# Kernel tuning notes

Measured on AMD Instinct MI355X. Metric: run time of the kernel, lower is better.

## Reference

```python
import jax, jax.numpy as jnp
import numpy as np

WD, WH, WW = 4, 8, 8
N_WIN = WD * WH * WW  # 256 tokens per window
NUM_HEADS = 8
DIM = 512
HIDDEN = int(DIM * 4.0)
SHIFT = (2, 4, 4)
EPS = 1e-5


def _rel_pos_index():
    coords = np.stack(np.meshgrid(np.arange(WD), np.arange(WH), np.arange(WW), indexing='ij'))
    cf = coords.reshape(3, -1)  # [3, N]
    rc = cf[:, :, None] - cf[:, None, :]  # [3, N, N]
    rc = rc.transpose(1, 2, 0).astype(np.int64)
    rc[:, :, 0] += WD - 1
    rc[:, :, 1] += WH - 1
    rc[:, :, 2] += WW - 1
    rc[:, :, 0] *= (2 * WH - 1) * (2 * WW - 1)
    rc[:, :, 1] *= (2 * WW - 1)
    return jnp.asarray(rc.sum(-1))  # [N, N]

REL_IDX = _rel_pos_index()


def setup_inputs() -> dict:
    key = jax.random.key(0)
    ks = jax.random.split(key, 10)
    B, D, H, W = 1, 16, 64, 64
    L = D * H * W
    s = 0.02
    table_size = (2 * WD - 1) * (2 * WH - 1) * (2 * WW - 1)  # 1575
    return {
        'x': jax.random.normal(ks[0], (B, L, DIM), jnp.float32),
        't_emb': jax.random.normal(ks[1], (B, DIM), jnp.float32),
        'ada_w': jax.random.normal(ks[2], (DIM, 6 * DIM), jnp.float32) * s,
        'ada_b': jnp.zeros((6 * DIM,), jnp.float32),
        'rel_table': jax.random.normal(ks[3], (table_size, NUM_HEADS), jnp.float32) * s,
        'qkv_w': jax.random.normal(ks[4], (DIM, 3 * DIM), jnp.float32) * s,
        'qkv_b': jnp.zeros((3 * DIM,), jnp.float32),
        'proj_w': jax.random.normal(ks[5], (DIM, DIM), jnp.float32) * s,
        'proj_b': jnp.zeros((DIM,), jnp.float32),
        'fc1_w': jax.random.normal(ks[6], (DIM, HIDDEN), jnp.float32) * s,
        'fc1_b': jnp.zeros((HIDDEN,), jnp.float32),
        'fc2_w': jax.random.normal(ks[7], (HIDDEN, DIM), jnp.float32) * s,
        'fc2_b': jnp.zeros((DIM,), jnp.float32),
        'D': D, 'H': H, 'W': W,
    }


def _layernorm(y):
    m = jnp.mean(y, axis=-1, keepdims=True)
    v = jnp.mean(jnp.square(y - m), axis=-1, keepdims=True)
    return (y - m) * jax.lax.rsqrt(v + EPS)


def _window_partition(x3, D, H, W):
    B, _, _, _, C = x3.shape
    x3 = x3.reshape(B, D // WD, WD, H // WH, WH, W // WW, WW, C)
    x3 = x3.transpose(0, 1, 3, 5, 2, 4, 6, 7)
    return x3.reshape(-1, N_WIN, C)


def _window_reverse(win, B, D, H, W):
    C = win.shape[-1]
    x3 = win.reshape(B, D // WD, H // WH, W // WW, WD, WH, WW, C)
    x3 = x3.transpose(0, 1, 4, 2, 5, 3, 6, 7)
    return x3.reshape(B, D, H, W, C)


def _window_attention(xn, rel_table, qkv_w, qkv_b, proj_w, proj_b):
    Bn, N, C = xn.shape
    h, d = NUM_HEADS, C // NUM_HEADS
    qkv = (xn @ qkv_w + qkv_b).reshape(Bn, N, 3, h, d).transpose(2, 0, 3, 1, 4)
    q, k, v = qkv[0], qkv[1], qkv[2]
    scale = d ** -0.5
    attn = jnp.einsum('bhnd,bhmd->bhnm', q * scale, k)  # [Bn, h, N, N]
    bias = rel_table[REL_IDX]  # gather -> [N, N, h]
    attn = jax.nn.softmax(attn + bias.transpose(2, 0, 1)[None], axis=-1)
    o = jnp.einsum('bhnm,bhmd->bhnd', attn, v)
    o = o.transpose(0, 2, 1, 3).reshape(Bn, N, C)
    return o @ proj_w + proj_b


def reference(x, t_emb, ada_w, ada_b, rel_table, qkv_w, qkv_b, proj_w, proj_b,
              fc1_w, fc1_b, fc2_w, fc2_b, D, H, W):
    B, L, C = x.shape
    mod = jax.nn.silu(t_emb) @ ada_w + ada_b  # [B, 6C]
    shift_msa, scale_msa, gate_msa, shift_mlp, scale_mlp, gate_mlp = jnp.split(mod, 6, axis=-1)

    x3 = x.reshape(B, D, H, W, C)
    x3 = jnp.roll(x3, shift=(-SHIFT[0], -SHIFT[1], -SHIFT[2]), axis=(1, 2, 3))
    xw = _window_partition(x3, D, H, W)  # [B*nW, N, C]

    xn = _layernorm(xw) * (1.0 + scale_msa[:, None, :]) + shift_msa[:, None, :]
    attn_out = _window_attention(xn, rel_table, qkv_w, qkv_b, proj_w, proj_b)
    xw = xw + gate_msa[:, None, :] * attn_out

    x3 = _window_reverse(xw, B, D, H, W)
    x3 = jnp.roll(x3, shift=SHIFT, axis=(1, 2, 3))
    x = x3.reshape(B, L, C)

    xn = _layernorm(x) * (1.0 + scale_mlp[:, None, :]) + shift_mlp[:, None, :]
    h1 = jax.nn.gelu(xn @ fc1_w + fc1_b, approximate=False)
    mlp_out = h1 @ fc2_w + fc2_b
    return x + gate_mlp[:, None, :] * mlp_out
```

## Files before the change

### kernel.cpp

```cpp
#include <hip/hip_runtime.h>
#include <hip/hip_bf16.h>
#include <math.h>


typedef __attribute__((ext_vector_type(8))) short short8;
typedef __attribute__((ext_vector_type(4))) short bs4;
typedef __attribute__((ext_vector_type(4))) float f32x4;

typedef const __attribute__((address_space(1))) unsigned int gu32;
typedef __attribute__((address_space(3))) unsigned int lu32;

__device__ __forceinline__ float bf2f(short s) {
  unsigned int u = ((unsigned int)(unsigned short)s) << 16;
  float f;
  __builtin_memcpy(&f, &u, 4);
  return f;
}
__device__ __forceinline__ short f2bf(float f) {
  unsigned int u;
  __builtin_memcpy(&u, &f, 4);
  u += 0x7FFFu + ((u >> 16) & 1u);
  return (short)(u >> 16);
}
__device__ __forceinline__ short f2bf_trunc(float f) {
  unsigned int u;
  __builtin_memcpy(&u, &f, 4);
  return (short)(u >> 16);
}

__device__ __forceinline__ int win_to_src(int p) {
  int wi = p >> 8, t = p & 255;
  int sd = (((wi >> 6) << 2) + (t >> 6) + 2) & 15;
  int sh = ((((wi >> 3) & 7) << 3) + ((t >> 3) & 7) + 4) & 63;
  int sw = (((wi & 7) << 3) + (t & 7) + 4) & 63;
  return (sd << 12) | (sh << 6) | sw;
}

__global__ __launch_bounds__(256) void mod_kernel(
    const float* __restrict__ t_emb, const float* __restrict__ ada_w,
    const float* __restrict__ ada_b, float* __restrict__ mod) {
  __shared__ float sl[512];
  int tid = threadIdx.x;
  for (int r = 0; r < 2; ++r) {
    float x = t_emb[r * 256 + tid];
    sl[r * 256 + tid] = x / (1.f + expf(-x));
  }
  __syncthreads();
  int col = blockIdx.x * 256 + tid;
  float acc = ada_b[col];
  for (int k = 0; k < 512; ++k)
    acc += sl[k] * ada_w[(size_t)k * 3072 + col];
  mod[col] = acc;
}

__global__ __launch_bounds__(256) void bias_kernel(
    const float* __restrict__ rel_table, short* __restrict__ biasT) {
  int head = blockIdx.x >> 8;
  int j = blockIdx.x & 255;
  int i = threadIdx.x;
  int di = i >> 6, hi = (i >> 3) & 7, wi = i & 7;
  int dj = j >> 6, hj = (j >> 3) & 7, wj = j & 7;
  int idx = (di - dj + 3) * 225 + (hi - hj + 7) * 15 + (wi - wj + 7);
  biasT[(size_t)blockIdx.x * 256 + i] = f2bf(rel_table[idx * 8 + head]);
}

__global__ __launch_bounds__(256) void perm_transpose_kernel(
    const float* __restrict__ in, short* __restrict__ out, int Nin, int K) {
  __shared__ float t[64][65];
  int a = blockIdx.x;
  int kb = blockIdx.y;
  int tx = threadIdx.x & 63, ty = threadIdx.x >> 6;
#pragma unroll
  for (int r = 0; r < 16; ++r) {
    int kk = ty * 16 + r;
    t[kk][tx] = in[(size_t)(kb * 64 + kk) * Nin + a * 64 + tx];
  }
  __syncthreads();
#pragma unroll
  for (int r = 0; r < 16; ++r) {
    int jl = ty * 16 + r;
    int lc = 4 * (jl & 15) + ((jl >> 4) & 3);
    out[(size_t)(a * 64 + jl) * K + kb * 64 + tx] = f2bf(t[tx][lc]);
  }
}

template <int GATHER>
__global__ __launch_bounds__(256) void ln_kernel(
    const float* __restrict__ xin, short* __restrict__ xout,
    const float* __restrict__ shv, const float* __restrict__ scv) {
  int wave = threadIdx.x >> 6, lane = threadIdx.x & 63;
  int p = blockIdx.x * 4 + wave;
  int s = GATHER ? win_to_src(p) : p;
  const f32x4* px = (const f32x4*)(xin + (size_t)s * 512 + lane * 8);
  f32x4 a = px[0], b = px[1];
  float xs[8];
#pragma unroll
  for (int j = 0; j < 4; ++j) { xs[j] = a[j]; xs[4 + j] = b[j]; }
  float sum = 0.f, sq = 0.f;
#pragma unroll
  for (int j = 0; j < 8; ++j) { sum += xs[j]; sq += xs[j] * xs[j]; }
#pragma unroll
  for (int off = 1; off < 64; off <<= 1) {
    sum += __shfl_xor(sum, off, 64);
    sq += __shfl_xor(sq, off, 64);
  }
  float mean = sum * (1.f / 512.f);
  float var = sq * (1.f / 512.f) - mean * mean;
  float rs = rsqrtf(var + 1e-5f);
  short8 o;
#pragma unroll
  for (int j = 0; j < 8; ++j) {
    int c = lane * 8 + j;
    float val = (xs[j] - mean) * rs * (1.f + scv[c]) + shv[c];
    o[j] = f2bf(val);
  }
  *(short8*)(xout + (size_t)p * 512 + lane * 8) = o;
}

template <int EPI>
__global__ __launch_bounds__(512) void gemm_kernel(
    const short* __restrict__ A, const short* __restrict__ BT,
    const float* __restrict__ bias, void* __restrict__ Cv,
    int M, int N, int K, int nbn,
    const float* __restrict__ resid, const float* __restrict__ gate) {
  __shared__ __align__(16) short Atl[256 * 64];
  __shared__ __align__(16) short Btl[128 * 64];

  int nwg = gridDim.x;
  int bid = blockIdx.x;
  int q = nwg >> 3, r = nwg & 7;
  int xcd = bid & 7, idx = bid >> 3;
  int swz = (xcd < r ? xcd * (q + 1) : r * (q + 1) + (xcd - r) * q) + idx;
  int bm = swz / nbn, bn = swz % nbn;

  int tid = threadIdx.x;
  int lane = tid & 63, wave = tid >> 6;
  int l15 = lane & 15, lg = lane >> 4;
  int wr = (wave >> 1) * 64, wc = (wave & 1) * 64;

  const size_t rowb = (size_t)K * 2;
  const char* ga[4];
  const char* gb[2];
  int loA[4], loB[2];
#pragma unroll
  for (int rr = 0; rr < 4; ++rr) {
    int o = rr * 8192 + tid * 16;
    int so = o ^ (((o >> 7) & 7) << 4);
    int row = so >> 7, cb = so & 127;
    loA[rr] = o;
    ga[rr] = (const char*)A + (size_t)(bm * 256 + row) * rowb + cb;
  }
#pragma unroll
  for (int rr = 0; rr < 2; ++rr) {
    int o = rr * 8192 + tid * 16;
    int so = o ^ (((o >> 7) & 7) << 4);
    int row = so >> 7, cb = so & 127;
    loB[rr] = o;
    gb[rr] = (const char*)BT + (size_t)(bn * 128 + row) * rowb + cb;
  }

  f32x4 acc[4][4];
#pragma unroll
  for (int m = 0; m < 4; ++m)
#pragma unroll
    for (int n = 0; n < 4; ++n) acc[m][n] = (f32x4){0.f, 0.f, 0.f, 0.f};

  const int swr = (l15 & 7) << 4;

  for (int kt = 0; kt < K; kt += 64) {
#pragma unroll
    for (int rr = 0; rr < 4; ++rr) {
      __builtin_amdgcn_global_load_lds((gu32*)ga[rr], (lu32*)((char*)Atl + loA[rr]), 16, 0, 0);
      ga[rr] += 128;
    }
#pragma unroll
    for (int rr = 0; rr < 2; ++rr) {
      __builtin_amdgcn_global_load_lds((gu32*)gb[rr], (lu32*)((char*)Btl + loB[rr]), 16, 0, 0);
      gb[rr] += 128;
    }
    __syncthreads();

    short8 af[2][4], bfr[2][4];
#pragma unroll
    for (int m = 0; m < 4; ++m) {
      int base = (wr + m * 16 + l15) * 128;
#pragma unroll
      for (int ks = 0; ks < 2; ++ks)
        af[ks][m] = *(const short8*)((const char*)Atl + base + ((ks * 64 + lg * 16) ^ swr));
    }
#pragma unroll
    for (int n = 0; n < 4; ++n) {
      int base = (wc + n * 16 + l15) * 128;
#pragma unroll
      for (int ks = 0; ks < 2; ++ks)
        bfr[ks][n] = *(const short8*)((const char*)Btl + base + ((ks * 64 + lg * 16) ^ swr));
    }
#pragma unroll
    for (int ks = 0; ks < 2; ++ks)
#pragma unroll
      for (int m = 0; m < 4; ++m)
#pragma unroll
        for (int n = 0; n < 4; ++n)
          acc[m][n] = __builtin_amdgcn_mfma_f32_16x16x32_bf16(af[ks][m], bfr[ks][n], acc[m][n], 0, 0, 0);
    __syncthreads();
  }

  int colb = bn * 128 + wc + 4 * l15;
  f32x4 bv4 = *(const f32x4*)(bias + colb);
  if (EPI == 0) {
    float sc = (colb < 512) ? 0.125f : 1.f;
#pragma unroll
    for (int m = 0; m < 4; ++m)
#pragma unroll
      for (int i = 0; i < 4; ++i) {
        int row = bm * 256 + wr + m * 16 + lg * 4 + i;
        bs4 pk;
#pragma unroll
        for (int n = 0; n < 4; ++n) pk[n] = f2bf_trunc((acc[m][n][i] + bv4[n]) * sc);
        *(bs4*)((short*)Cv + (size_t)row * N + colb) = pk;
      }
  } else if (EPI == 1) {
#pragma unroll
    for (int m = 0; m < 4; ++m)
#pragma unroll
      for (int i = 0; i < 4; ++i) {
        int row = bm * 256 + wr + m * 16 + lg * 4 + i;
        bs4 pk;
#pragma unroll
        for (int n = 0; n < 4; ++n) {
          float v = acc[m][n][i] + bv4[n];
          float tt = v * (0.7978845608f + 0.0356774081f * v * v);
          float sg = 1.f / (1.f + __expf(-2.f * tt));
          pk[n] = f2bf_trunc(v * sg);
        }
        *(bs4*)((short*)Cv + (size_t)row * N + colb) = pk;
      }
  } else {
    f32x4 gv = *(const f32x4*)(gate + colb);
#pragma unroll
    for (int m = 0; m < 4; ++m)
#pragma unroll
      for (int i = 0; i < 4; ++i) {
        int row = bm * 256 + wr + m * 16 + lg * 4 + i;
        int s = (EPI == 2) ? win_to_src(row) : row;
        f32x4 rv = *(const f32x4*)(resid + (size_t)s * 512 + colb);
        f32x4 o;
#pragma unroll
        for (int n = 0; n < 4; ++n) o[n] = rv[n] + gv[n] * (acc[m][n][i] + bv4[n]);
        *(f32x4*)((float*)Cv + (size_t)s * 512 + colb) = o;
      }
  }
}

__global__ __launch_bounds__(512) void attn_kernel(
    const short* __restrict__ qkv, const short* __restrict__ biasT,
    short* __restrict__ aout) {
  __shared__ __align__(16) short vt[64][264];
  __shared__ __align__(16) short pl[8][32][40];
  int win = blockIdx.x, head = blockIdx.y;
  int tid = threadIdx.x, lane = tid & 63, wave = tid >> 6;
  int l15 = lane & 15, lg = lane >> 4;
  const short* qp = qkv + (size_t)win * 256 * 1536 + head * 64;
  const short* kp = qp + 512;
  const short* vp = qp + 1024;

  int key = tid >> 1, dh = (tid & 1) * 32;
#pragma unroll
  for (int r = 0; r < 4; ++r) {
    short8 vv = *(const short8*)(vp + (size_t)key * 1536 + dh + r * 8);
#pragma unroll
    for (int j = 0; j < 8; ++j) vt[dh + r * 8 + j][key] = vv[j];
  }

  short8 qf[2][2];
#pragma unroll
  for (int m = 0; m < 2; ++m)
#pragma unroll
    for (int kk = 0; kk < 2; ++kk)
      qf[m][kk] = *(const short8*)(qp + (size_t)(wave * 32 + m * 16 + l15) * 1536 + kk * 32 + lg * 8);

  __syncthreads();

  float lsum[2][4];
  f32x4 ao[2][4];
#pragma unroll
  for (int m = 0; m < 2; ++m)
#pragma unroll
    for (int i = 0; i < 4; ++i) lsum[m][i] = 0.f;
#pragma unroll
  for (int m = 0; m < 2; ++m)
#pragma unroll
    for (int n = 0; n < 4; ++n) ao[m][n] = (f32x4){0.f, 0.f, 0.f, 0.f};

  for (int kc = 0; kc < 4; ++kc) {
    f32x4 sv[2][4];
#pragma unroll
    for (int m = 0; m < 2; ++m)
#pragma unroll
      for (int n = 0; n < 4; ++n) sv[m][n] = (f32x4){0.f, 0.f, 0.f, 0.f};
#pragma unroll
    for (int n = 0; n < 4; ++n)
#pragma unroll
      for (int kk = 0; kk < 2; ++kk) {
        short8 kf = *(const short8*)(kp + (size_t)(kc * 64 + n * 16 + l15) * 1536 + kk * 32 + lg * 8);
#pragma unroll
        for (int m = 0; m < 2; ++m)
          sv[m][n] = __builtin_amdgcn_mfma_f32_16x16x32_bf16(qf[m][kk], kf, sv[m][n], 0, 0, 0);
      }
#pragma unroll
    for (int n = 0; n < 4; ++n) {
      const short* bq = biasT + (size_t)(head * 256 + kc * 64 + n * 16 + l15) * 256 + wave * 32 + lg * 4;
#pragma unroll
      for (int m = 0; m < 2; ++m) {
        bs4 bt = *(const bs4*)(bq + m * 16);
#pragma unroll
        for (int i = 0; i < 4; ++i) {
          float pe = __expf(sv[m][n][i] + bf2f(bt[i]));
          sv[m][n][i] = pe;
          lsum[m][i] += pe;
        }
      }
    }
#pragma unroll
    for (int s = 0; s < 2; ++s) {
#pragma unroll
      for (int m = 0; m < 2; ++m)
#pragma unroll
        for (int nn = 0; nn < 2; ++nn) {
          int n = 2 * s + nn;
#pragma unroll
          for (int i = 0; i < 4; ++i)
            pl[wave][m * 16 + lg * 4 + i][nn * 16 + l15] = f2bf_trunc(sv[m][n][i]);
        }
      short8 pf[2];
#pragma unroll
      for (int m = 0; m < 2; ++m)
        pf[m] = *(const short8*)&pl[wave][m * 16 + l15][lg * 8];
#pragma unroll
      for (int n2 = 0; n2 < 4; ++n2) {
        short8 vf = *(const short8*)&vt[n2 * 16 + l15][kc * 64 + s * 32 + lg * 8];
#pragma unroll
        for (int m = 0; m < 2; ++m)
          ao[m][n2] = __builtin_amdgcn_mfma_f32_16x16x32_bf16(pf[m], vf, ao[m][n2], 0, 0, 0);
      }
    }
  }

#pragma unroll
  for (int m = 0; m < 2; ++m)
#pragma unroll
    for (int i = 0; i < 4; ++i) {
#pragma unroll
      for (int off = 1; off < 16; off <<= 1)
        lsum[m][i] += __shfl_xor(lsum[m][i], off, 64);
    }

#pragma unroll
  for (int m = 0; m < 2; ++m)
#pragma unroll
    for (int i = 0; i < 4; ++i) {
      float inv = 1.f / lsum[m][i];
      int row = win * 256 + wave * 32 + m * 16 + lg * 4 + i;
#pragma unroll
      for (int n = 0; n < 4; ++n)
        aout[(size_t)row * 512 + head * 64 + n * 16 + l15] = f2bf(ao[m][n][i] * inv);
    }
}

extern "C" void kernel_launch(void* const* d_in, const int* in_sizes, int n_in,
                              void* d_out, int out_size, void* d_ws, size_t ws_size,
                              hipStream_t stream) {
  (void)in_sizes; (void)n_in; (void)out_size; (void)ws_size;
  const float* x         = (const float*)d_in[0];
  const float* t_emb     = (const float*)d_in[1];
  const float* ada_w     = (const float*)d_in[2];
  const float* ada_b     = (const float*)d_in[3];
  const float* rel_table = (const float*)d_in[4];
  const float* qkv_w     = (const float*)d_in[5];
  const float* qkv_b     = (const float*)d_in[6];
  const float* proj_w    = (const float*)d_in[7];
  const float* proj_b    = (const float*)d_in[8];
  const float* fc1_w     = (const float*)d_in[9];
  const float* fc1_b     = (const float*)d_in[10];
  const float* fc2_w     = (const float*)d_in[11];
  const float* fc2_b     = (const float*)d_in[12];
  float* out = (float*)d_out;
  char* ws = (char*)d_ws;

  float* mod    = (float*)(ws);
  short* biasT  = (short*)(ws + 16384);
  short* qkvwT  = (short*)(ws + 16384 + 2097152);
  short* projwT = qkvwT + 1536 * 512;
  short* fc1wT  = projwT + 512 * 512;
  short* fc2wT  = fc1wT + 2048 * 512;
  short* xn     = (short*)(ws + 8404992);
  short* qkvb   = xn + (size_t)65536 * 512;
  short* attno  = qkvb + (size_t)65536 * 1536;
  short* h1     = qkvb;
  float* x2     = out;

  mod_kernel<<<12, 256, 0, stream>>>(t_emb, ada_w, ada_b, mod);
  bias_kernel<<<2048, 256, 0, stream>>>(rel_table, biasT);
  perm_transpose_kernel<<<dim3(24, 8), 256, 0, stream>>>(qkv_w, qkvwT, 1536, 512);
  perm_transpose_kernel<<<dim3(8, 8), 256, 0, stream>>>(proj_w, projwT, 512, 512);
  perm_transpose_kernel<<<dim3(32, 8), 256, 0, stream>>>(fc1_w, fc1wT, 2048, 512);
  perm_transpose_kernel<<<dim3(8, 32), 256, 0, stream>>>(fc2_w, fc2wT, 512, 2048);

  ln_kernel<1><<<16384, 256, 0, stream>>>(x, xn, mod + 0, mod + 512);
  gemm_kernel<0><<<256 * 12, 512, 0, stream>>>(xn, qkvwT, qkv_b, qkvb,
                                               65536, 1536, 512, 12, nullptr, nullptr);
  attn_kernel<<<dim3(256, 8), 512, 0, stream>>>(qkvb, biasT, attno);
  gemm_kernel<2><<<256 * 4, 512, 0, stream>>>(attno, projwT, proj_b, x2,
                                              65536, 512, 512, 4, x, mod + 1024);
  ln_kernel<0><<<16384, 256, 0, stream>>>(x2, xn, mod + 1536, mod + 2048);
  gemm_kernel<1><<<256 * 16, 512, 0, stream>>>(xn, fc1wT, fc1_b, h1,
                                               65536, 2048, 512, 16, nullptr, nullptr);
  gemm_kernel<3><<<256 * 4, 512, 0, stream>>>(h1, fc2wT, fc2_b, out,
                                              65536, 512, 2048, 4, x2, mod + 2560);
}
```

Measured before the change: 846.1 us.

## Double-buffer GEMM LDS tiles with K=32 stages and async prefetch

The GEMM main loop now uses two LDS buffers of half the K depth (32 instead of 64). Global-to-LDS loads for tile t+2 are issued while MFMAs run on tile t, with explicit vmcnt/lgkmcnt waits and barriers. This is meant to hide global memory latency behind compute instead of serialising load-then-compute. The cost is smaller k-steps, which means more barriers per unit of work, and a re-derived XOR swizzle for 64-byte rows that may cause LDS bank conflicts.

```diff
diff --git a/kernel.cpp b/kernel.cpp
--- a/kernel.cpp
+++ b/kernel.cpp
@@ -123,8 +123,8 @@
     const float* __restrict__ bias, void* __restrict__ Cv,
     int M, int N, int K, int nbn,
     const float* __restrict__ resid, const float* __restrict__ gate) {
-  __shared__ __align__(16) short Atl[256 * 64];
-  __shared__ __align__(16) short Btl[128 * 64];
+  __shared__ __align__(16) short Atl[2][256 * 32];
+  __shared__ __align__(16) short Btl[2][128 * 32];
 
   int nwg = gridDim.x;
   int bid = blockIdx.x;
@@ -139,24 +139,21 @@
   int wr = (wave >> 1) * 64, wc = (wave & 1) * 64;
 
   const size_t rowb = (size_t)K * 2;
-  const char* ga[4];
-  const char* gb[2];
-  int loA[4], loB[2];
-#pragma unroll
-  for (int rr = 0; rr < 4; ++rr) {
-    int o = rr * 8192 + tid * 16;
-    int so = o ^ (((o >> 7) & 7) << 4);
-    int row = so >> 7, cb = so & 127;
-    loA[rr] = o;
-    ga[rr] = (const char*)A + (size_t)(bm * 256 + row) * rowb + cb;
-  }
+  const char* ga[2];
+  const char* gb;
+  int loA[2], loB;
 #pragma unroll
   for (int rr = 0; rr < 2; ++rr) {
     int o = rr * 8192 + tid * 16;
-    int so = o ^ (((o >> 7) & 7) << 4);
-    int row = so >> 7, cb = so & 127;
-    loB[rr] = o;
-    gb[rr] = (const char*)BT + (size_t)(bn * 128 + row) * rowb + cb;
+    int so = o ^ (((o >> 6) & 3) << 4);
+    loA[rr] = o;
+    ga[rr] = (const char*)A + (size_t)(bm * 256 + (so >> 6)) * rowb + (so & 63);
+  }
+  {
+    int o = tid * 16;
+    int so = o ^ (((o >> 6) & 3) << 4);
+    loB = o;
+    gb = (const char*)BT + (size_t)(bn * 128 + (so >> 6)) * rowb + (so & 63);
   }
 
   f32x4 acc[4][4];
@@ -165,44 +162,60 @@
 #pragma unroll
     for (int n = 0; n < 4; ++n) acc[m][n] = (f32x4){0.f, 0.f, 0.f, 0.f};
 
-  const int swr = (l15 & 7) << 4;
-
-  for (int kt = 0; kt < K; kt += 64) {
-#pragma unroll
-    for (int rr = 0; rr < 4; ++rr) {
-      __builtin_amdgcn_global_load_lds((gu32*)ga[rr], (lu32*)((char*)Atl + loA[rr]), 16, 0, 0);
-      ga[rr] += 128;
-    }
-#pragma unroll
-    for (int rr = 0; rr < 2; ++rr) {
-      __builtin_amdgcn_global_load_lds((gu32*)gb[rr], (lu32*)((char*)Btl + loB[rr]), 16, 0, 0);
-      gb[rr] += 128;
-    }
-    __syncthreads();
-
-    short8 af[2][4], bfr[2][4];
-#pragma unroll
-    for (int m = 0; m < 4; ++m) {
-      int base = (wr + m * 16 + l15) * 128;
-#pragma unroll
-      for (int ks = 0; ks < 2; ++ks)
-        af[ks][m] = *(const short8*)((const char*)Atl + base + ((ks * 64 + lg * 16) ^ swr));
-    }
-#pragma unroll
-    for (int n = 0; n < 4; ++n) {
-      int base = (wc + n * 16 + l15) * 128;
-#pragma unroll
-      for (int ks = 0; ks < 2; ++ks)
-        bfr[ks][n] = *(const short8*)((const char*)Btl + base + ((ks * 64 + lg * 16) ^ swr));
-    }
-#pragma unroll
-    for (int ks = 0; ks < 2; ++ks)
-#pragma unroll
-      for (int m = 0; m < 4; ++m)
-#pragma unroll
-        for (int n = 0; n < 4; ++n)
-          acc[m][n] = __builtin_amdgcn_mfma_f32_16x16x32_bf16(af[ks][m], bfr[ks][n], acc[m][n], 0, 0, 0);
-    __syncthreads();
+  const int swr = (l15 & 3) << 4;
+
+  auto stage = [&](int buf) {
+    __builtin_amdgcn_global_load_lds((gu32*)ga[0], (lu32*)((char*)Atl[buf] + loA[0]), 16, 0, 0);
+    __builtin_amdgcn_global_load_lds((gu32*)ga[1], (lu32*)((char*)Atl[buf] + loA[1]), 16, 0, 0);
+    __builtin_amdgcn_global_load_lds((gu32*)gb,    (lu32*)((char*)Btl[buf] + loB),    16, 0, 0);
+    ga[0] += 64; ga[1] += 64; gb += 64;
+  };
+
+  const int nt = K >> 5;
+  stage(0);
+  stage(1);
+  int c = 0;
+  for (int t = 0; t < nt - 1; ++t) {
+    asm volatile("s_waitcnt vmcnt(3)" ::: "memory");
+    __builtin_amdgcn_sched_barrier(0);
+    __builtin_amdgcn_s_barrier();
+    __builtin_amdgcn_sched_barrier(0);
+    short8 af[4], bfr[4];
+#pragma unroll
+    for (int m = 0; m < 4; ++m)
+      af[m] = *(const short8*)((const char*)Atl[c] + (wr + m * 16 + l15) * 64 + (lg * 16 ^ swr));
+#pragma unroll
+    for (int n = 0; n < 4; ++n)
+      bfr[n] = *(const short8*)((const char*)Btl[c] + (wc + n * 16 + l15) * 64 + (lg * 16 ^ swr));
+    asm volatile("s_waitcnt lgkmcnt(0)" ::: "memory");
+    __builtin_amdgcn_sched_barrier(0);
+    __builtin_amdgcn_s_barrier();
+    __builtin_amdgcn_sched_barrier(0);
+    if (t + 2 < nt) stage(c);
+#pragma unroll
+    for (int m = 0; m < 4; ++m)
+#pragma unroll
+      for (int n = 0; n < 4; ++n)
+        acc[m][n] = __builtin_amdgcn_mfma_f32_16x16x32_bf16(af[m], bfr[n], acc[m][n], 0, 0, 0);
+    c ^= 1;
+  }
+  asm volatile("s_waitcnt vmcnt(0)" ::: "memory");
+  __builtin_amdgcn_sched_barrier(0);
+  __builtin_amdgcn_s_barrier();
+  __builtin_amdgcn_sched_barrier(0);
+  {
+    short8 af[4], bfr[4];
+#pragma unroll
+    for (int m = 0; m < 4; ++m)
+      af[m] = *(const short8*)((const char*)Atl[c] + (wr + m * 16 + l15) * 64 + (lg * 16 ^ swr));
+#pragma unroll
+    for (int n = 0; n < 4; ++n)
+      bfr[n] = *(const short8*)((const char*)Btl[c] + (wc + n * 16 + l15) * 64 + (lg * 16 ^ swr));
+#pragma unroll
+    for (int m = 0; m < 4; ++m)
+#pragma unroll
+      for (int n = 0; n < 4; ++n)
+        acc[m][n] = __builtin_amdgcn_mfma_f32_16x16x32_bf16(af[m], bfr[n], acc[m][n], 0, 0, 0);
   }
 
   int colb = bn * 128 + wc + 4 * l15;
```

Result: slower. 864.4 us (+2.2%).

## Double-buffer GEMM LDS tiles and enlarge block tile to 256x256

Applied to the files above, without the earlier changes.

The GEMM kernel now keeps two LDS buffers and issues global-to-LDS loads for the next K tile while computing the current one, with one barrier per iteration instead of two. The block tile grows from 256x128 to 256x256, so each wave computes a 128x64 sub-tile with 32 accumulators, and the grids are halved to match. This aims to hide load latency and raise data reuse per LDS byte. In exchange it uses 128KB of LDS and more registers per block, which limits occupancy, and the 512-wide GEMMs now launch only 512 blocks.

```diff
diff --git a/kernel.cpp b/kernel.cpp
--- a/kernel.cpp
+++ b/kernel.cpp
@@ -118,13 +118,13 @@
 }
 
 template <int EPI>
-__global__ __launch_bounds__(512) void gemm_kernel(
+__global__ __launch_bounds__(512, 2) void gemm_kernel(
     const short* __restrict__ A, const short* __restrict__ BT,
     const float* __restrict__ bias, void* __restrict__ Cv,
     int M, int N, int K, int nbn,
     const float* __restrict__ resid, const float* __restrict__ gate) {
-  __shared__ __align__(16) short Atl[256 * 64];
-  __shared__ __align__(16) short Btl[128 * 64];
+  __shared__ __align__(16) short Atl[2][256 * 64];
+  __shared__ __align__(16) short Btl[2][256 * 64];
 
   int nwg = gridDim.x;
   int bid = blockIdx.x;
@@ -136,99 +136,109 @@
   int tid = threadIdx.x;
   int lane = tid & 63, wave = tid >> 6;
   int l15 = lane & 15, lg = lane >> 4;
-  int wr = (wave >> 1) * 64, wc = (wave & 1) * 64;
+  int wr = (wave >> 2) * 128;
+  int wc = (wave & 3) * 64;
 
   const size_t rowb = (size_t)K * 2;
   const char* ga[4];
-  const char* gb[2];
-  int loA[4], loB[2];
+  const char* gb[4];
+  int lo[4];
 #pragma unroll
   for (int rr = 0; rr < 4; ++rr) {
     int o = rr * 8192 + tid * 16;
     int so = o ^ (((o >> 7) & 7) << 4);
     int row = so >> 7, cb = so & 127;
-    loA[rr] = o;
+    lo[rr] = o;
     ga[rr] = (const char*)A + (size_t)(bm * 256 + row) * rowb + cb;
-  }
-#pragma unroll
-  for (int rr = 0; rr < 2; ++rr) {
-    int o = rr * 8192 + tid * 16;
-    int so = o ^ (((o >> 7) & 7) << 4);
-    int row = so >> 7, cb = so & 127;
-    loB[rr] = o;
-    gb[rr] = (const char*)BT + (size_t)(bn * 128 + row) * rowb + cb;
-  }
-
-  f32x4 acc[4][4];
-#pragma unroll
-  for (int m = 0; m < 4; ++m)
+    gb[rr] = (const char*)BT + (size_t)(bn * 256 + row) * rowb + cb;
+  }
+
+  f32x4 acc[8][4];
+#pragma unroll
+  for (int m = 0; m < 8; ++m)
 #pragma unroll
     for (int n = 0; n < 4; ++n) acc[m][n] = (f32x4){0.f, 0.f, 0.f, 0.f};
 
   const int swr = (l15 & 7) << 4;
 
-  for (int kt = 0; kt < K; kt += 64) {
+  auto stage = [&](int buf) {
 #pragma unroll
     for (int rr = 0; rr < 4; ++rr) {
-      __builtin_amdgcn_global_load_lds((gu32*)ga[rr], (lu32*)((char*)Atl + loA[rr]), 16, 0, 0);
+      __builtin_amdgcn_global_load_lds((gu32*)ga[rr], (lu32*)((char*)Atl[buf] + lo[rr]), 16, 0, 0);
       ga[rr] += 128;
     }
 #pragma unroll
-    for (int rr = 0; rr < 2; ++rr) {
-      __builtin_amdgcn_global_load_lds((gu32*)gb[rr], (lu32*)((char*)Btl + loB[rr]), 16, 0, 0);
+    for (int rr = 0; rr < 4; ++rr) {
+      __builtin_amdgcn_global_load_lds((gu32*)gb[rr], (lu32*)((char*)Btl[buf] + lo[rr]), 16, 0, 0);
       gb[rr] += 128;
     }
-    __syncthreads();
-
-    short8 af[2][4], bfr[2][4];
-#pragma unroll
-    for (int m = 0; m < 4; ++m) {
-      int base = (wr + m * 16 + l15) * 128;
-#pragma unroll
-      for (int ks = 0; ks < 2; ++ks)
-        af[ks][m] = *(const short8*)((const char*)Atl + base + ((ks * 64 + lg * 16) ^ swr));
-    }
+  };
+
+  const int nt = K >> 6;
+  stage(0);
+  asm volatile("s_waitcnt vmcnt(0)" ::: "memory");
+  __builtin_amdgcn_sched_barrier(0);
+  __builtin_amdgcn_s_barrier();
+  int c = 0;
+  for (int t = 0; t < nt; ++t) {
+    if (t + 1 < nt) stage(c ^ 1);
+    short8 bfr[4][2];
 #pragma unroll
     for (int n = 0; n < 4; ++n) {
       int base = (wc + n * 16 + l15) * 128;
 #pragma unroll
       for (int ks = 0; ks < 2; ++ks)
-        bfr[ks][n] = *(const short8*)((const char*)Btl + base + ((ks * 64 + lg * 16) ^ swr));
-    }
-#pragma unroll
-    for (int ks = 0; ks < 2; ++ks)
-#pragma unroll
-      for (int m = 0; m < 4; ++m)
-#pragma unroll
-        for (int n = 0; n < 4; ++n)
-          acc[m][n] = __builtin_amdgcn_mfma_f32_16x16x32_bf16(af[ks][m], bfr[ks][n], acc[m][n], 0, 0, 0);
-    __syncthreads();
-  }
-
-  int colb = bn * 128 + wc + 4 * l15;
+        bfr[n][ks] = *(const short8*)((const char*)Btl[c] + base + ((ks * 64 + lg * 16) ^ swr));
+    }
+#pragma unroll
+    for (int mh = 0; mh < 2; ++mh) {
+      short8 af[4][2];
+#pragma unroll
+      for (int m = 0; m < 4; ++m) {
+        int base = (wr + mh * 64 + m * 16 + l15) * 128;
+#pragma unroll
+        for (int ks = 0; ks < 2; ++ks)
+          af[m][ks] = *(const short8*)((const char*)Atl[c] + base + ((ks * 64 + lg * 16) ^ swr));
+      }
+#pragma unroll
+      for (int ks = 0; ks < 2; ++ks)
+#pragma unroll
+        for (int m = 0; m < 4; ++m)
+#pragma unroll
+          for (int n = 0; n < 4; ++n)
+            acc[mh * 4 + m][n] =
+                __builtin_amdgcn_mfma_f32_16x16x32_bf16(af[m][ks], bfr[n][ks], acc[mh * 4 + m][n], 0, 0, 0);
+    }
+    asm volatile("s_waitcnt vmcnt(0)" ::: "memory");
+    __builtin_amdgcn_sched_barrier(0);
+    __builtin_amdgcn_s_barrier();
+    c ^= 1;
+  }
+
+  int colb = bn * 256 + wc + 4 * l15;
   f32x4 bv4 = *(const f32x4*)(bias + colb);
   if (EPI == 0) {
     float sc = (colb < 512) ? 0.125f : 1.f;
 #pragma unroll
-    for (int m = 0; m < 4; ++m)
+    for (int mf = 0; mf < 8; ++mf)
 #pragma unroll
       for (int i = 0; i < 4; ++i) {
-        int row = bm * 256 + wr + m * 16 + lg * 4 + i;
+        int row = bm * 256 + wr + (mf >> 2) * 64 + (mf & 3) * 16 + lg * 4 + i;
         bs4 pk;
 #pragma unroll
-        for (int n = 0; n < 4; ++n) pk[n] = f2bf_trunc((acc[m][n][i] + bv4[n]) * sc);
+        for (int n = 0; n < 4; ++n) pk[n] = f2bf_trunc((acc[mf][n][i] + bv4[n]) * sc);
         *(bs4*)((short*)Cv + (size_t)row * N + colb) = pk;
       }
   } else if (EPI == 1) {
 #pragma unroll
-    for (int m = 0; m < 4; ++m)
+    for (int mf = 0; mf < 8; ++mf)
 #pragma unroll
       for (int i = 0; i < 4; ++i) {
-        int row = bm * 256 + wr + m * 16 + lg * 4 + i;
+        int row = bm * 256 + wr + (mf >> 2) * 64 + (mf & 3) * 16 + lg * 4 + i;
         bs4 pk;
 #pragma unroll
         for (int n = 0; n < 4; ++n) {
-          float v = acc[m][n][i] + bv4[n];
+          float v = acc[mf][n][i] + bv4[n];
           float tt = v * (0.7978845608f + 0.0356774081f * v * v);
           float sg = 1.f / (1.f + __expf(-2.f * tt));
           pk[n] = f2bf_trunc(v * sg);
@@ -238,15 +248,15 @@
   } else {
     f32x4 gv = *(const f32x4*)(gate + colb);
 #pragma unroll
-    for (int m = 0; m < 4; ++m)
+    for (int mf = 0; mf < 8; ++mf)
 #pragma unroll
       for (int i = 0; i < 4; ++i) {
-        int row = bm * 256 + wr + m * 16 + lg * 4 + i;
+        int row = bm * 256 + wr + (mf >> 2) * 64 + (mf & 3) * 16 + lg * 4 + i;
         int s = (EPI == 2) ? win_to_src(row) : row;
         f32x4 rv = *(const f32x4*)(resid + (size_t)s * 512 + colb);
         f32x4 o;
 #pragma unroll
-        for (int n = 0; n < 4; ++n) o[n] = rv[n] + gv[n] * (acc[m][n][i] + bv4[n]);
+        for (int n = 0; n < 4; ++n) o[n] = rv[n] + gv[n] * (acc[mf][n][i] + bv4[n]);
         *(f32x4*)((float*)Cv + (size_t)s * 512 + colb) = o;
       }
   }
@@ -407,14 +417,14 @@
   perm_transpose_kernel<<<dim3(8, 32), 256, 0, stream>>>(fc2_w, fc2wT, 512, 2048);
 
   ln_kernel<1><<<16384, 256, 0, stream>>>(x, xn, mod + 0, mod + 512);
-  gemm_kernel<0><<<256 * 12, 512, 0, stream>>>(xn, qkvwT, qkv_b, qkvb,
-                                               65536, 1536, 512, 12, nullptr, nullptr);
+  gemm_kernel<0><<<256 * 6, 512, 0, stream>>>(xn, qkvwT, qkv_b, qkvb,
+                                              65536, 1536, 512, 6, nullptr, nullptr);
   attn_kernel<<<dim3(256, 8), 512, 0, stream>>>(qkvb, biasT, attno);
-  gemm_kernel<2><<<256 * 4, 512, 0, stream>>>(attno, projwT, proj_b, x2,
-                                              65536, 512, 512, 4, x, mod + 1024);
+  gemm_kernel<2><<<256 * 2, 512, 0, stream>>>(attno, projwT, proj_b, x2,
+                                              65536, 512, 512, 2, x, mod + 1024);
   ln_kernel<0><<<16384, 256, 0, stream>>>(x2, xn, mod + 1536, mod + 2048);
-  gemm_kernel<1><<<256 * 16, 512, 0, stream>>>(xn, fc1wT, fc1_b, h1,
-                                               65536, 2048, 512, 16, nullptr, nullptr);
-  gemm_kernel<3><<<256 * 4, 512, 0, stream>>>(h1, fc2wT, fc2_b, out,
-                                              65536, 512, 2048, 4, x2, mod + 2560);
-}
+  gemm_kernel<1><<<256 * 8, 512, 0, stream>>>(xn, fc1wT, fc1_b, h1,
+                                              65536, 2048, 512, 8, nullptr, nullptr);
+  gemm_kernel<3><<<256 * 2, 512, 0, stream>>>(h1, fc2wT, fc2_b, out,
+                                              65536, 512, 2048, 2, x2, mod + 2560);
+}
```

Measured after the change: 912.5 us. +7.8%, slower.

## Stream A operand from global and stage whole-K weight panel in LDS

Applied to the files above, without the earlier changes.

Replaces the 256x128 double-operand LDS-tiled GEMM with a 512x64 tile in which each wave reads its A rows straight from global memory into registers. Only the B (weight) panel, up to 512 of K wide, is loaded into swizzled LDS, once per K chunk. This is meant to cut LDS traffic and barriers per K step. In exchange, A loads are no longer shared through LDS, the N tile is narrower so A is re-read across more column blocks, and global load latency is exposed with no prefetch.

```diff
diff --git a/kernel.cpp b/kernel.cpp
--- a/kernel.cpp
+++ b/kernel.cpp
@@ -117,14 +117,13 @@
   *(short8*)(xout + (size_t)p * 512 + lane * 8) = o;
 }
 
-template <int EPI>
-__global__ __launch_bounds__(512) void gemm_kernel(
+template <int EPI, int KCH>
+__global__ __launch_bounds__(512) void gemm_stream_kernel(
     const short* __restrict__ A, const short* __restrict__ BT,
     const float* __restrict__ bias, void* __restrict__ Cv,
     int M, int N, int K, int nbn,
     const float* __restrict__ resid, const float* __restrict__ gate) {
-  __shared__ __align__(16) short Atl[256 * 64];
-  __shared__ __align__(16) short Btl[128 * 64];
+  __shared__ __align__(16) short Bs[64 * 512];
 
   int nwg = gridDim.x;
   int bid = blockIdx.x;
@@ -136,28 +135,23 @@
   int tid = threadIdx.x;
   int lane = tid & 63, wave = tid >> 6;
   int l15 = lane & 15, lg = lane >> 4;
-  int wr = (wave >> 1) * 64, wc = (wave & 1) * 64;
 
   const size_t rowb = (size_t)K * 2;
-  const char* ga[4];
-  const char* gb[2];
-  int loA[4], loB[2];
-#pragma unroll
-  for (int rr = 0; rr < 4; ++rr) {
+
+  const char* gB[8];
+  int loB[8];
+#pragma unroll
+  for (int rr = 0; rr < 8; ++rr) {
     int o = rr * 8192 + tid * 16;
-    int so = o ^ (((o >> 7) & 7) << 4);
-    int row = so >> 7, cb = so & 127;
-    loA[rr] = o;
-    ga[rr] = (const char*)A + (size_t)(bm * 256 + row) * rowb + cb;
-  }
-#pragma unroll
-  for (int rr = 0; rr < 2; ++rr) {
-    int o = rr * 8192 + tid * 16;
-    int so = o ^ (((o >> 7) & 7) << 4);
-    int row = so >> 7, cb = so & 127;
+    int so = o ^ (((o >> 10) & 7) << 4);
     loB[rr] = o;
-    gb[rr] = (const char*)BT + (size_t)(bn * 128 + row) * rowb + cb;
-  }
+    gB[rr] = (const char*)BT + (size_t)(bn * 64 + (so >> 10)) * rowb + (so & 1023);
+  }
+
+  const char* pA[4];
+#pragma unroll
+  for (int m = 0; m < 4; ++m)
+    pA[m] = (const char*)A + (size_t)(bm * 512 + wave * 64 + m * 16 + l15) * rowb + lg * 16;
 
   f32x4 acc[4][4];
 #pragma unroll
@@ -167,45 +161,33 @@
 
   const int swr = (l15 & 7) << 4;
 
-  for (int kt = 0; kt < K; kt += 64) {
-#pragma unroll
-    for (int rr = 0; rr < 4; ++rr) {
-      __builtin_amdgcn_global_load_lds((gu32*)ga[rr], (lu32*)((char*)Atl + loA[rr]), 16, 0, 0);
-      ga[rr] += 128;
+  for (int kc = 0; kc < KCH; ++kc) {
+    if (kc) __syncthreads();
+#pragma unroll
+    for (int rr = 0; rr < 8; ++rr)
+      __builtin_amdgcn_global_load_lds((gu32*)(gB[rr] + kc * 1024),
+                                       (lu32*)((char*)Bs + loB[rr]), 16, 0, 0);
+    __syncthreads();
+
+#pragma unroll 4
+    for (int ks = 0; ks < 16; ++ks) {
+      short8 af[4], bfr[4];
+#pragma unroll
+      for (int m = 0; m < 4; ++m)
+        af[m] = *(const short8*)(pA[m] + kc * 1024 + ks * 64);
+#pragma unroll
+      for (int n = 0; n < 4; ++n)
+        bfr[n] = *(const short8*)((const char*)Bs + (n * 16 + l15) * 1024 +
+                                  ((ks * 64 + lg * 16) ^ swr));
+#pragma unroll
+      for (int m = 0; m < 4; ++m)
+#pragma unroll
+        for (int n = 0; n < 4; ++n)
+          acc[m][n] = __builtin_amdgcn_mfma_f32_16x16x32_bf16(af[m], bfr[n], acc[m][n], 0, 0, 0);
     }
-#pragma unroll
-    for (int rr = 0; rr < 2; ++rr) {
-      __builtin_amdgcn_global_load_lds((gu32*)gb[rr], (lu32*)((char*)Btl + loB[rr]), 16, 0, 0);
-      gb[rr] += 128;
-    }
-    __syncthreads();
-
-    short8 af[2][4], bfr[2][4];
-#pragma unroll
-    for (int m = 0; m < 4; ++m) {
-      int base = (wr + m * 16 + l15) * 128;
-#pragma unroll
-      for (int ks = 0; ks < 2; ++ks)
-        af[ks][m] = *(const short8*)((const char*)Atl + base + ((ks * 64 + lg * 16) ^ swr));
-    }
-#pragma unroll
-    for (int n = 0; n < 4; ++n) {
-      int base = (wc + n * 16 + l15) * 128;
-#pragma unroll
-      for (int ks = 0; ks < 2; ++ks)
-        bfr[ks][n] = *(const short8*)((const char*)Btl + base + ((ks * 64 + lg * 16) ^ swr));
-    }
-#pragma unroll
-    for (int ks = 0; ks < 2; ++ks)
-#pragma unroll
-      for (int m = 0; m < 4; ++m)
-#pragma unroll
-        for (int n = 0; n < 4; ++n)
-          acc[m][n] = __builtin_amdgcn_mfma_f32_16x16x32_bf16(af[ks][m], bfr[ks][n], acc[m][n], 0, 0, 0);
-    __syncthreads();
-  }
-
-  int colb = bn * 128 + wc + 4 * l15;
+  }
+
+  int colb = bn * 64 + 4 * l15;
   f32x4 bv4 = *(const f32x4*)(bias + colb);
   if (EPI == 0) {
     float sc = (colb < 512) ? 0.125f : 1.f;
@@ -213,7 +195,7 @@
     for (int m = 0; m < 4; ++m)
 #pragma unroll
       for (int i = 0; i < 4; ++i) {
-        int row = bm * 256 + wr + m * 16 + lg * 4 + i;
+        int row = bm * 512 + wave * 64 + m * 16 + lg * 4 + i;
         bs4 pk;
 #pragma unroll
         for (int n = 0; n < 4; ++n) pk[n] = f2bf_trunc((acc[m][n][i] + bv4[n]) * sc);
@@ -224,7 +206,7 @@
     for (int m = 0; m < 4; ++m)
 #pragma unroll
       for (int i = 0; i < 4; ++i) {
-        int row = bm * 256 + wr + m * 16 + lg * 4 + i;
+        int row = bm * 512 + wave * 64 + m * 16 + lg * 4 + i;
         bs4 pk;
 #pragma unroll
         for (int n = 0; n < 4; ++n) {
@@ -241,7 +223,7 @@
     for (int m = 0; m < 4; ++m)
 #pragma unroll
       for (int i = 0; i < 4; ++i) {
-        int row = bm * 256 + wr + m * 16 + lg * 4 + i;
+        int row = bm * 512 + wave * 64 + m * 16 + lg * 4 + i;
         int s = (EPI == 2) ? win_to_src(row) : row;
         f32x4 rv = *(const f32x4*)(resid + (size_t)s * 512 + colb);
         f32x4 o;
@@ -407,14 +389,14 @@
   perm_transpose_kernel<<<dim3(8, 32), 256, 0, stream>>>(fc2_w, fc2wT, 512, 2048);
 
   ln_kernel<1><<<16384, 256, 0, stream>>>(x, xn, mod + 0, mod + 512);
-  gemm_kernel<0><<<256 * 12, 512, 0, stream>>>(xn, qkvwT, qkv_b, qkvb,
-                                               65536, 1536, 512, 12, nullptr, nullptr);
+  gemm_stream_kernel<0, 1><<<128 * 24, 512, 0, stream>>>(
+      xn, qkvwT, qkv_b, qkvb, 65536, 1536, 512, 24, nullptr, nullptr);
   attn_kernel<<<dim3(256, 8), 512, 0, stream>>>(qkvb, biasT, attno);
-  gemm_kernel<2><<<256 * 4, 512, 0, stream>>>(attno, projwT, proj_b, x2,
-                                              65536, 512, 512, 4, x, mod + 1024);
+  gemm_stream_kernel<2, 1><<<128 * 8, 512, 0, stream>>>(
+      attno, projwT, proj_b, x2, 65536, 512, 512, 8, x, mod + 1024);
   ln_kernel<0><<<16384, 256, 0, stream>>>(x2, xn, mod + 1536, mod + 2048);
-  gemm_kernel<1><<<256 * 16, 512, 0, stream>>>(xn, fc1wT, fc1_b, h1,
-                                               65536, 2048, 512, 16, nullptr, nullptr);
-  gemm_kernel<3><<<256 * 4, 512, 0, stream>>>(h1, fc2wT, fc2_b, out,
-                                              65536, 512, 2048, 4, x2, mod + 2560);
-}
+  gemm_stream_kernel<1, 1><<<128 * 32, 512, 0, stream>>>(
+      xn, fc1wT, fc1_b, h1, 65536, 2048, 512, 32, nullptr, nullptr);
+  gemm_stream_kernel<3, 4><<<128 * 8, 512, 0, stream>>>(
+      h1, fc2wT, fc2_b, out, 65536, 512, 2048, 8, x2, mod + 2560);
+}
```

Result: slower. 1.220 ms (+44.2%).
